# Performance work log

Hardware: AMD Instinct MI355X
Metric: run time of the kernel (lower is better)

The kernel has to match this reference:

```python
import jax, jax.numpy as jnp
import numpy as np

N, F, E, D, H, G = 65536, 256, 16, 256, 512, 256  # nodes, feat, experts(node_num), emb_dim, hidden_dim, graphs


def setup_inputs() -> dict:
    key = jax.random.key(0)
    ks = jax.random.split(key, 11)
    scale = 0.02
    return {
        "node_fea": jax.random.normal(ks[0], (N, F), jnp.float32),
        "masks": jax.random.uniform(ks[1], (N, F), jnp.float32),
        "node_type": jax.random.randint(ks[2], (N,), 0, E),
        "g_node_id": jnp.sort(jax.random.randint(ks[3], (G,), 0, N)),
        "label": jax.random.randint(ks[4], (G,), 0, 2),
        "W_emb": jax.random.normal(ks[5], (E, F, D), jnp.float32) * scale,
        "b_emb": jax.random.normal(ks[6], (E, D), jnp.float32) * scale,
        "W_hid": jax.random.normal(ks[7], (D, H), jnp.float32) * scale,
        "b_hid": jax.random.normal(ks[8], (H,), jnp.float32) * scale,
        "W_out": jax.random.normal(ks[9], (H, 2), jnp.float32) * scale,
        "b_out": jax.random.normal(ks[10], (2,), jnp.float32) * scale,
    }


def reference(node_fea, masks, node_type, g_node_id, label,
              W_emb, b_emb, W_hid, b_hid, W_out, b_out):
    # --- node_embedding: per-node type-routed linear (grouped GEMM form) ---
    xm = node_fea * masks                                   # [N, F]
    # run every expert densely, then select each node's expert output
    all_emb = jnp.einsum('nf,efd->ned', xm, W_emb) + b_emb[None]   # [N, E, D]
    emb = jnp.take_along_axis(all_emb, node_type[:, None, None], axis=1)[:, 0, :]  # [N, D]
    # --- hidden_fc (dropout in eval mode = identity) ---
    h = emb @ W_hid + b_hid                                 # [N, H]
    # --- pick first node of each batched graph ---
    g_emb = h[g_node_id]                                    # [G, H]
    # --- output layer: Linear + Softmax ---
    probs = jax.nn.softmax(g_emb @ W_out + b_out, axis=-1)  # [G, 2]
    # --- CrossEntropyLoss(reduction='sum') applied to probs (as in source) ---
    logp = jax.nn.log_softmax(probs, axis=-1)
    loss = -jnp.sum(jnp.take_along_axis(logp, label[:, None], axis=1))
    return probs, loss
```

## Files before the change

kernel.cpp:

```cpp
#include <hip/hip_runtime.h>
#include <math.h>

#define NN 65536
#define FF 256
#define EE 16
#define DD 256
#define HH 512
#define GG 256
#define NBLK 64


__device__ __forceinline__ void grid_barrier(int* c, int target) {
    __syncthreads();
    if (threadIdx.x == 0) {
        __hip_atomic_fetch_add(c, 1, __ATOMIC_ACQ_REL, __HIP_MEMORY_SCOPE_AGENT);
        while (__hip_atomic_load(c, __ATOMIC_ACQUIRE, __HIP_MEMORY_SCOPE_AGENT)
               < target) {
            __builtin_amdgcn_s_sleep(1);
        }
    }
    __syncthreads();
}

__global__ __launch_bounds__(256) void fused_all_kernel(
    const float* __restrict__ node_fea,
    const float* __restrict__ masks,
    const int*   __restrict__ node_type,
    const int*   __restrict__ g_node_id,
    const int*   __restrict__ label,
    const float* __restrict__ W_emb,
    const float* __restrict__ b_emb,
    const float* __restrict__ W_hid,
    const float* __restrict__ b_hid,
    const float* __restrict__ W_out,
    const float* __restrict__ b_out,
    float* __restrict__ out,
    float* __restrict__ ws_f,
    int*   __restrict__ ws_i)
{
    __shared__ __align__(16) float lwtmp[2 * DD];

    const int t = threadIdx.x;
    const int b = blockIdx.x;
    const int w = t >> 6;
    const int l = t & 63;

    float* wtmp   = ws_f + 16;
    float* bconst = ws_f + 528;
    float* lterm  = ws_f + 544;
    float* fold   = ws_f + 1024;

    const int g = (b << 2) + w;
    const int n = g_node_id[g];
    const int e = node_type[n];
    const size_t nb = (size_t)n * FF + (l << 2);
    const float4 x4  = *(const float4*)(node_fea + nb);
    const float4 m4  = *(const float4*)(masks + nb);
    const float4 be4 = *(const float4*)(b_emb + e * DD + (l << 2));

    {
        const int d = (b << 2) + w;
        const float* Wr = W_hid + (size_t)d * HH + (l << 3);
        const float4 h0 = *(const float4*)(Wr);
        const float4 h1 = *(const float4*)(Wr + 4);
        const float* Wo = W_out + (l << 4);
        const float4 o0 = *(const float4*)(Wo);
        const float4 o1 = *(const float4*)(Wo + 4);
        const float4 o2 = *(const float4*)(Wo + 8);
        const float4 o3 = *(const float4*)(Wo + 12);
        float a0 = h0.x*o0.x + h0.y*o0.z + h0.z*o1.x + h0.w*o1.z
                 + h1.x*o2.x + h1.y*o2.z + h1.z*o3.x + h1.w*o3.z;
        float a1 = h0.x*o0.y + h0.y*o0.w + h0.z*o1.y + h0.w*o1.w
                 + h1.x*o2.y + h1.y*o2.w + h1.z*o3.y + h1.w*o3.w;
        float c0 = 0.f, c1 = 0.f;
        if (b == 0 && w == 0) {
            const float4 bh0 = *(const float4*)(b_hid + (l << 3));
            const float4 bh1 = *(const float4*)(b_hid + (l << 3) + 4);
            c0 = bh0.x*o0.x + bh0.y*o0.z + bh0.z*o1.x + bh0.w*o1.z
               + bh1.x*o2.x + bh1.y*o2.z + bh1.z*o3.x + bh1.w*o3.z;
            c1 = bh0.x*o0.y + bh0.y*o0.w + bh0.z*o1.y + bh0.w*o1.w
               + bh1.x*o2.y + bh1.y*o2.w + bh1.z*o3.y + bh1.w*o3.w;
        }
        for (int off = 32; off; off >>= 1) {
            a0 += __shfl_down(a0, off, 64);
            a1 += __shfl_down(a1, off, 64);
            c0 += __shfl_down(c0, off, 64);
            c1 += __shfl_down(c1, off, 64);
        }
        if (l == 0) {
            wtmp[2 * d]     = a0;
            wtmp[2 * d + 1] = a1;
            if (b == 0 && w == 0) {
                bconst[0] = c0 + b_out[0];
                bconst[1] = c1 + b_out[1];
            }
        }
    }
    grid_barrier(ws_i + 0, NBLK);

    {
        *(float2*)(lwtmp + 2 * t) = *(const float2*)(wtmp + 2 * t);
        __syncthreads();

        const int e2  = b >> 2;
        const int r   = b & 3;
        const int row = (r << 6) + (t >> 2);
        const int d0  = (t & 3) << 6;
        const float* We = W_emb + ((size_t)e2 * FF + row) * DD + d0;
        float z0 = 0.f, z1 = 0.f;
        #pragma unroll 4
        for (int i = 0; i < 16; ++i) {
            const float4 wv = *(const float4*)(We + 4 * i);
            const int d2 = 2 * (d0 + 4 * i);
            z0 = fmaf(wv.x, lwtmp[d2 + 0], z0);  z1 = fmaf(wv.x, lwtmp[d2 + 1], z1);
            z0 = fmaf(wv.y, lwtmp[d2 + 2], z0);  z1 = fmaf(wv.y, lwtmp[d2 + 3], z1);
            z0 = fmaf(wv.z, lwtmp[d2 + 4], z0);  z1 = fmaf(wv.z, lwtmp[d2 + 5], z1);
            z0 = fmaf(wv.w, lwtmp[d2 + 6], z0);  z1 = fmaf(wv.w, lwtmp[d2 + 7], z1);
        }
        z0 += __shfl_xor(z0, 1, 64);  z1 += __shfl_xor(z1, 1, 64);
        z0 += __shfl_xor(z0, 2, 64);  z1 += __shfl_xor(z1, 2, 64);
        if ((t & 3) == 0)
            *(float2*)(fold + ((size_t)e2 * FF + row) * 2) = (float2){z0, z1};
    }
    grid_barrier(ws_i + 1, NBLK);

    {
        const float* fr = fold + e * (FF * 2) + (l << 3);
        const float4 wa  = *(const float4*)(fr);
        const float4 wb  = *(const float4*)(fr + 4);
        const float4 wt0 = *(const float4*)(wtmp + (l << 3));
        const float4 wt1 = *(const float4*)(wtmp + (l << 3) + 4);
        const float x0 = x4.x * m4.x, x1 = x4.y * m4.y;
        const float x2 = x4.z * m4.z, x3 = x4.w * m4.w;
        float z0 = x0*wa.x + x1*wa.z + x2*wb.x + x3*wb.z
                 + be4.x*wt0.x + be4.y*wt0.z + be4.z*wt1.x + be4.w*wt1.z;
        float z1 = x0*wa.y + x1*wa.w + x2*wb.y + x3*wb.w
                 + be4.x*wt0.y + be4.y*wt0.w + be4.z*wt1.y + be4.w*wt1.w;
        for (int off = 32; off; off >>= 1) {
            z0 += __shfl_down(z0, off, 64);
            z1 += __shfl_down(z1, off, 64);
        }
        if (l == 0) {
            z0 += bconst[0];
            z1 += bconst[1];
            const float mz = fmaxf(z0, z1);
            const float e0 = expf(z0 - mz), e1 = expf(z1 - mz);
            const float inv = 1.0f / (e0 + e1);
            const float p0 = e0 * inv, p1 = e1 * inv;
            out[2 * g + 0] = p0;
            out[2 * g + 1] = p1;
            const float mp  = fmaxf(p0, p1);
            const float lse = mp + logf(expf(p0 - mp) + expf(p1 - mp));
            lterm[g] = lse - ((label[g] == 0) ? p0 : p1);
        }
    }
    grid_barrier(ws_i + 2, NBLK);

    if (b == 0 && t < 64) {
        float v = lterm[t] + lterm[t + 64] + lterm[t + 128] + lterm[t + 192];
        for (int off = 32; off; off >>= 1) v += __shfl_down(v, off, 64);
        if (t == 0) out[2 * GG] = v;
    }
}

extern "C" void kernel_launch(void* const* d_in, const int* in_sizes, int n_in,
                              void* d_out, int out_size, void* d_ws, size_t ws_size,
                              hipStream_t stream) {
    const float* node_fea  = (const float*)d_in[0];
    const float* masks     = (const float*)d_in[1];
    const int*   node_type = (const int*)  d_in[2];
    const int*   g_node_id = (const int*)  d_in[3];
    const int*   label     = (const int*)  d_in[4];
    const float* W_emb     = (const float*)d_in[5];
    const float* b_emb     = (const float*)d_in[6];
    const float* W_hid     = (const float*)d_in[7];
    const float* b_hid     = (const float*)d_in[8];
    const float* W_out     = (const float*)d_in[9];
    const float* b_out     = (const float*)d_in[10];

    float* out  = (float*)d_out;
    float* ws_f = (float*)d_ws;
    int*   ws_i = (int*)d_ws;

    hipMemsetAsync(d_ws, 0, 16, stream);

    fused_all_kernel<<<NBLK, 256, 0, stream>>>(
        node_fea, masks, node_type, g_node_id, label,
        W_emb, b_emb, W_hid, b_hid, W_out, b_out,
        out, ws_f, ws_i);
}
```

Before: 156.4 us.

## Split fused grid-barrier kernel into two launches with per-graph expert GEMV

The single 64-block kernel with three software grid barriers is replaced by two kernels. A small kernel folds W_hid·W_out into a 256x2 matrix and resets the counter, replacing the memset. A 256-block kernel then computes each graph's expert embedding directly as a GEMV over that node's W_emb slice and finishes with a last-block atomic reduction for the loss. This removes the spin-wait barriers and the fold of all 16 experts, but each graph block now reads a full 256 KB expert matrix, which relies on L2 reuse across blocks that share an expert.

Measured after the change: 154.2 us. Within noise of the previous version (-1.4%).

```diff
diff --git a/kernel.cpp b/kernel.cpp
--- a/kernel.cpp
+++ b/kernel.cpp
@@ -7,22 +7,66 @@
 #define DD 256
 #define HH 512
 #define GG 256
-#define NBLK 64
 
 
-__device__ __forceinline__ void grid_barrier(int* c, int target) {
-    __syncthreads();
-    if (threadIdx.x == 0) {
-        __hip_atomic_fetch_add(c, 1, __ATOMIC_ACQ_REL, __HIP_MEMORY_SCOPE_AGENT);
-        while (__hip_atomic_load(c, __ATOMIC_ACQUIRE, __HIP_MEMORY_SCOPE_AGENT)
-               < target) {
-            __builtin_amdgcn_s_sleep(1);
+__global__ __launch_bounds__(256) void wtmp_kernel(
+    const float* __restrict__ W_hid,
+    const float* __restrict__ b_hid,
+    const float* __restrict__ W_out,
+    const float* __restrict__ b_out,
+    float* __restrict__ ws_f,
+    int*   __restrict__ ws_i)
+{
+    const int t = threadIdx.x;
+    const int b = blockIdx.x;
+    const int w = t >> 6;
+    const int l = t & 63;
+
+    float* wtmp   = ws_f + 16;
+    float* bconst = ws_f + 528;
+
+    if (b == 0 && t == 0) ws_i[0] = 0;
+
+    const int d = (b << 2) + w;
+    const float* Wr = W_hid + (size_t)d * HH + (l << 3);
+    const float4 h0 = *(const float4*)(Wr);
+    const float4 h1 = *(const float4*)(Wr + 4);
+    const float* Wo = W_out + (l << 4);
+    const float4 o0 = *(const float4*)(Wo);
+    const float4 o1 = *(const float4*)(Wo + 4);
+    const float4 o2 = *(const float4*)(Wo + 8);
+    const float4 o3 = *(const float4*)(Wo + 12);
+    float a0 = h0.x*o0.x + h0.y*o0.z + h0.z*o1.x + h0.w*o1.z
+             + h1.x*o2.x + h1.y*o2.z + h1.z*o3.x + h1.w*o3.z;
+    float a1 = h0.x*o0.y + h0.y*o0.w + h0.z*o1.y + h0.w*o1.w
+             + h1.x*o2.y + h1.y*o2.w + h1.z*o3.y + h1.w*o3.w;
+
+    float c0 = 0.f, c1 = 0.f;
+    if (b == 0 && w == 0) {
+        const float4 bh0 = *(const float4*)(b_hid + (l << 3));
+        const float4 bh1 = *(const float4*)(b_hid + (l << 3) + 4);
+        c0 = bh0.x*o0.x + bh0.y*o0.z + bh0.z*o1.x + bh0.w*o1.z
+           + bh1.x*o2.x + bh1.y*o2.z + bh1.z*o3.x + bh1.w*o3.z;
+        c1 = bh0.x*o0.y + bh0.y*o0.w + bh0.z*o1.y + bh0.w*o1.w
+           + bh1.x*o2.y + bh1.y*o2.w + bh1.z*o3.y + bh1.w*o3.w;
+    }
+    for (int off = 32; off; off >>= 1) {
+        a0 += __shfl_down(a0, off, 64);
+        a1 += __shfl_down(a1, off, 64);
+        c0 += __shfl_down(c0, off, 64);
+        c1 += __shfl_down(c1, off, 64);
+    }
+    if (l == 0) {
+        wtmp[2 * d]     = a0;
+        wtmp[2 * d + 1] = a1;
+        if (b == 0 && w == 0) {
+            bconst[0] = c0 + b_out[0];
+            bconst[1] = c1 + b_out[1];
         }
     }
-    __syncthreads();
 }
 
-__global__ __launch_bounds__(256) void fused_all_kernel(
+__global__ __launch_bounds__(256) void graph_kernel(
     const float* __restrict__ node_fea,
     const float* __restrict__ masks,
     const int*   __restrict__ node_type,
@@ -30,136 +74,93 @@
     const int*   __restrict__ label,
     const float* __restrict__ W_emb,
     const float* __restrict__ b_emb,
-    const float* __restrict__ W_hid,
-    const float* __restrict__ b_hid,
-    const float* __restrict__ W_out,
-    const float* __restrict__ b_out,
     float* __restrict__ out,
     float* __restrict__ ws_f,
     int*   __restrict__ ws_i)
 {
-    __shared__ __align__(16) float lwtmp[2 * DD];
+    __shared__ __align__(16) float xm[FF];
+    __shared__ __align__(16) float part[4][DD];
+    __shared__ float red0[4];
+    __shared__ float red1[4];
+    __shared__ int lastflag;
 
+    const int g = blockIdx.x;
     const int t = threadIdx.x;
-    const int b = blockIdx.x;
     const int w = t >> 6;
     const int l = t & 63;
-
-    float* wtmp   = ws_f + 16;
-    float* bconst = ws_f + 528;
-    float* lterm  = ws_f + 544;
-    float* fold   = ws_f + 1024;
-
-    const int g = (b << 2) + w;
+    const int c = l << 2;
     const int n = g_node_id[g];
     const int e = node_type[n];
-    const size_t nb = (size_t)n * FF + (l << 2);
-    const float4 x4  = *(const float4*)(node_fea + nb);
-    const float4 m4  = *(const float4*)(masks + nb);
-    const float4 be4 = *(const float4*)(b_emb + e * DD + (l << 2));
+
+    const float* wtmp   = ws_f + 16;
+    const float* bconst = ws_f + 528;
+    float*       lterm  = ws_f + 544;
 
     {
-        const int d = (b << 2) + w;
-        const float* Wr = W_hid + (size_t)d * HH + (l << 3);
-        const float4 h0 = *(const float4*)(Wr);
-        const float4 h1 = *(const float4*)(Wr + 4);
-        const float* Wo = W_out + (l << 4);
-        const float4 o0 = *(const float4*)(Wo);
-        const float4 o1 = *(const float4*)(Wo + 4);
-        const float4 o2 = *(const float4*)(Wo + 8);
-        const float4 o3 = *(const float4*)(Wo + 12);
-        float a0 = h0.x*o0.x + h0.y*o0.z + h0.z*o1.x + h0.w*o1.z
-                 + h1.x*o2.x + h1.y*o2.z + h1.z*o3.x + h1.w*o3.z;
-        float a1 = h0.x*o0.y + h0.y*o0.w + h0.z*o1.y + h0.w*o1.w
-                 + h1.x*o2.y + h1.y*o2.w + h1.z*o3.y + h1.w*o3.w;
-        float c0 = 0.f, c1 = 0.f;
-        if (b == 0 && w == 0) {
-            const float4 bh0 = *(const float4*)(b_hid + (l << 3));
-            const float4 bh1 = *(const float4*)(b_hid + (l << 3) + 4);
-            c0 = bh0.x*o0.x + bh0.y*o0.z + bh0.z*o1.x + bh0.w*o1.z
-               + bh1.x*o2.x + bh1.y*o2.z + bh1.z*o3.x + bh1.w*o3.z;
-            c1 = bh0.x*o0.y + bh0.y*o0.w + bh0.z*o1.y + bh0.w*o1.w
-               + bh1.x*o2.y + bh1.y*o2.w + bh1.z*o3.y + bh1.w*o3.w;
-        }
-        for (int off = 32; off; off >>= 1) {
-            a0 += __shfl_down(a0, off, 64);
-            a1 += __shfl_down(a1, off, 64);
-            c0 += __shfl_down(c0, off, 64);
-            c1 += __shfl_down(c1, off, 64);
-        }
-        if (l == 0) {
-            wtmp[2 * d]     = a0;
-            wtmp[2 * d + 1] = a1;
-            if (b == 0 && w == 0) {
-                bconst[0] = c0 + b_out[0];
-                bconst[1] = c1 + b_out[1];
-            }
-        }
+        const size_t base = (size_t)n * FF + t;
+        xm[t] = node_fea[base] * masks[base];
     }
-    grid_barrier(ws_i + 0, NBLK);
+    __syncthreads();
 
     {
-        *(float2*)(lwtmp + 2 * t) = *(const float2*)(wtmp + 2 * t);
-        __syncthreads();
+        const float* __restrict__ Wb = W_emb + (size_t)e * FF * DD;
+        float4 acc = {0.f, 0.f, 0.f, 0.f};
+        #pragma unroll 8
+        for (int i = 0; i < 64; ++i) {
+            const int f = (w << 6) + i;
+            const float s = xm[f];
+            const float4 wv = *(const float4*)(Wb + (size_t)f * DD + c);
+            acc.x = fmaf(s, wv.x, acc.x);
+            acc.y = fmaf(s, wv.y, acc.y);
+            acc.z = fmaf(s, wv.z, acc.z);
+            acc.w = fmaf(s, wv.w, acc.w);
+        }
+        *(float4*)&part[w][c] = acc;
+    }
+    __syncthreads();
 
-        const int e2  = b >> 2;
-        const int r   = b & 3;
-        const int row = (r << 6) + (t >> 2);
-        const int d0  = (t & 3) << 6;
-        const float* We = W_emb + ((size_t)e2 * FF + row) * DD + d0;
-        float z0 = 0.f, z1 = 0.f;
-        #pragma unroll 4
-        for (int i = 0; i < 16; ++i) {
-            const float4 wv = *(const float4*)(We + 4 * i);
-            const int d2 = 2 * (d0 + 4 * i);
-            z0 = fmaf(wv.x, lwtmp[d2 + 0], z0);  z1 = fmaf(wv.x, lwtmp[d2 + 1], z1);
-            z0 = fmaf(wv.y, lwtmp[d2 + 2], z0);  z1 = fmaf(wv.y, lwtmp[d2 + 3], z1);
-            z0 = fmaf(wv.z, lwtmp[d2 + 4], z0);  z1 = fmaf(wv.z, lwtmp[d2 + 5], z1);
-            z0 = fmaf(wv.w, lwtmp[d2 + 6], z0);  z1 = fmaf(wv.w, lwtmp[d2 + 7], z1);
+    float z0p, z1p;
+    {
+        const float embt = part[0][t] + part[1][t] + part[2][t] + part[3][t]
+                         + b_emb[e * DD + t];
+        const float2 wt = *(const float2*)(wtmp + 2 * t);
+        z0p = embt * wt.x;
+        z1p = embt * wt.y;
+    }
+    for (int off = 32; off; off >>= 1) {
+        z0p += __shfl_down(z0p, off, 64);
+        z1p += __shfl_down(z1p, off, 64);
+    }
+    if (l == 0) { red0[w] = z0p; red1[w] = z1p; }
+    __syncthreads();
+
+    if (t == 0) {
+        float z0 = bconst[0] + red0[0] + red0[1] + red0[2] + red0[3];
+        float z1 = bconst[1] + red1[0] + red1[1] + red1[2] + red1[3];
+        const float mz = fmaxf(z0, z1);
+        const float e0 = expf(z0 - mz), e1 = expf(z1 - mz);
+        const float inv = 1.0f / (e0 + e1);
+        const float p0 = e0 * inv, p1 = e1 * inv;
+        out[2 * g + 0] = p0;
+        out[2 * g + 1] = p1;
+        const float mp  = fmaxf(p0, p1);
+        const float lse = mp + logf(expf(p0 - mp) + expf(p1 - mp));
+        lterm[g] = lse - ((label[g] == 0) ? p0 : p1);
+        __threadfence();
+        const int old = __hip_atomic_fetch_add(ws_i, 1, __ATOMIC_ACQ_REL,
+                                               __HIP_MEMORY_SCOPE_AGENT);
+        lastflag = (old == GG - 1);
+    }
+    __syncthreads();
+
+    if (lastflag) {
+        __threadfence();
+        if (t < 64) {
+            const volatile float* lt = lterm;
+            float v = lt[t] + lt[t + 64] + lt[t + 128] + lt[t + 192];
+            for (int off = 32; off; off >>= 1) v += __shfl_down(v, off, 64);
+            if (t == 0) out[2 * GG] = v;
         }
-        z0 += __shfl_xor(z0, 1, 64);  z1 += __shfl_xor(z1, 1, 64);
-        z0 += __shfl_xor(z0, 2, 64);  z1 += __shfl_xor(z1, 2, 64);
-        if ((t & 3) == 0)
-            *(float2*)(fold + ((size_t)e2 * FF + row) * 2) = (float2){z0, z1};
-    }
-    grid_barrier(ws_i + 1, NBLK);
-
-    {
-        const float* fr = fold + e * (FF * 2) + (l << 3);
-        const float4 wa  = *(const float4*)(fr);
-        const float4 wb  = *(const float4*)(fr + 4);
-        const float4 wt0 = *(const float4*)(wtmp + (l << 3));
-        const float4 wt1 = *(const float4*)(wtmp + (l << 3) + 4);
-        const float x0 = x4.x * m4.x, x1 = x4.y * m4.y;
-        const float x2 = x4.z * m4.z, x3 = x4.w * m4.w;
-        float z0 = x0*wa.x + x1*wa.z + x2*wb.x + x3*wb.z
-                 + be4.x*wt0.x + be4.y*wt0.z + be4.z*wt1.x + be4.w*wt1.z;
-        float z1 = x0*wa.y + x1*wa.w + x2*wb.y + x3*wb.w
-                 + be4.x*wt0.y + be4.y*wt0.w + be4.z*wt1.y + be4.w*wt1.w;
-        for (int off = 32; off; off >>= 1) {
-            z0 += __shfl_down(z0, off, 64);
-            z1 += __shfl_down(z1, off, 64);
-        }
-        if (l == 0) {
-            z0 += bconst[0];
-            z1 += bconst[1];
-            const float mz = fmaxf(z0, z1);
-            const float e0 = expf(z0 - mz), e1 = expf(z1 - mz);
-            const float inv = 1.0f / (e0 + e1);
-            const float p0 = e0 * inv, p1 = e1 * inv;
-            out[2 * g + 0] = p0;
-            out[2 * g + 1] = p1;
-            const float mp  = fmaxf(p0, p1);
-            const float lse = mp + logf(expf(p0 - mp) + expf(p1 - mp));
-            lterm[g] = lse - ((label[g] == 0) ? p0 : p1);
-        }
-    }
-    grid_barrier(ws_i + 2, NBLK);
-
-    if (b == 0 && t < 64) {
-        float v = lterm[t] + lterm[t + 64] + lterm[t + 128] + lterm[t + 192];
-        for (int off = 32; off; off >>= 1) v += __shfl_down(v, off, 64);
-        if (t == 0) out[2 * GG] = v;
     }
 }
 
@@ -182,10 +183,10 @@
     float* ws_f = (float*)d_ws;
     int*   ws_i = (int*)d_ws;
 
-    hipMemsetAsync(d_ws, 0, 16, stream);
+    wtmp_kernel<<<64, 256, 0, stream>>>(
+        W_hid, b_hid, W_out, b_out, ws_f, ws_i);
 
-    fused_all_kernel<<<NBLK, 256, 0, stream>>>(
+    graph_kernel<<<GG, 256, 0, stream>>>(
         node_fea, masks, node_type, g_node_id, label,
-        W_emb, b_emb, W_hid, b_hid, W_out, b_out,
-        out, ws_f, ws_i);
+        W_emb, b_emb, out, ws_f, ws_i);
 }
```
